# Optimization experiments

Measured on AMD Instinct MI355X. Metric: run time of the kernel, lower is better.

Reference implementation:

```python
import jax, jax.numpy as jnp
import numpy as np

B, N, C, H = 4, 1025, 768, 12
KEEP_RATIO = 0.25
BETA = 1.0


def setup_inputs() -> dict:
    key = jax.random.key(0)
    k1, k2, k3, k4, k5 = jax.random.split(key, 5)
    x = jax.random.normal(k1, (B, N, C), dtype=jnp.float32)
    ucb_count_score = jax.random.uniform(k2, (H, N), dtype=jnp.float32)
    W_qkv = jax.random.normal(k3, (C, 3 * C), dtype=jnp.float32) * 0.02
    W_proj = jax.random.normal(k4, (C, C), dtype=jnp.float32) * 0.02
    b_proj = jax.random.normal(k5, (C,), dtype=jnp.float32) * 0.02
    return {"x": x, "ucb_count_score": ucb_count_score, "W_qkv": W_qkv,
            "W_proj": W_proj, "b_proj": b_proj, "counter": 100, "ucb_enabled": 1}


def reference(x, ucb_count_score, W_qkv, W_proj, b_proj, counter, ucb_enabled):
    Bn, Nn, Cn = x.shape
    Dh = Cn // H
    scale = Dh ** -0.5
    # qkv projection (no bias, qkv_bias=False)
    qkv = (x @ W_qkv).reshape(Bn, Nn, 3, H, Dh)
    q = jnp.transpose(qkv[:, :, 0], (0, 2, 1, 3))  # [B,H,N,Dh]
    k = jnp.transpose(qkv[:, :, 1], (0, 2, 1, 3))
    v = jnp.transpose(qkv[:, :, 2], (0, 2, 1, 3))
    attn_probs = jax.nn.softmax(jnp.einsum('bhnd,bhmd->bhnm', q, k) * scale, axis=-1)

    if ucb_enabled and counter > 50:
        # UCB pruning path (exclude_cls=True, keep_ratio set)
        total_patches = Nn - 1
        k_sel = max(1, int(total_patches * KEEP_RATIO))
        patch_scores = attn_probs[:, :, :, 1:].mean(axis=2)  # [B,H,N-1]
        expl = BETA * jnp.sqrt(jnp.log(counter + 1.0) / (ucb_count_score[:, 1:] + 1e-6))  # [H,N-1]
        global_ucb = (patch_scores + expl[None]).mean(axis=1)  # [B,N-1]
        _, sel = jax.lax.top_k(global_ucb, k_sel)  # [B,k]
        tok = sel + 1  # shift for CLS
        # keep[b,j] = 1 if token j is CLS or selected in batch b
        keep = jnp.zeros((Bn, Nn), dtype=attn_probs.dtype)
        keep = keep.at[jnp.arange(Bn)[:, None], tok].set(1.0).at[:, 0].set(1.0)
        # mask[b,h,i,j] = keep[b,i] OR keep[b,j]
        mask = jnp.maximum(keep[:, None, :, None], keep[:, None, None, :])
        pruned = attn_probs * mask
        pruned = pruned / (pruned.sum(axis=-1, keepdims=True) + 1e-8)
        context = jnp.einsum('bhnm,bhmd->bhnd', pruned, v)
        cnt = jnp.zeros((Nn,), dtype=jnp.float32).at[tok.reshape(-1)].add(1.0) / Bn
        score_delta = jnp.broadcast_to(cnt[None, :], ucb_count_score.shape)
    else:
        context = jnp.einsum('bhnm,bhmd->bhnd', attn_probs, v)
        score_delta = None

    out = context.transpose(0, 2, 1, 3).reshape(Bn, Nn, Cn) @ W_proj + b_proj
    return out, score_delta
```

## Files before the change

### kernel.cpp

```cpp
#include <hip/hip_runtime.h>
#include <hip/hip_bf16.h>
#include <math.h>

#define Bb 4
#define Nn 1025
#define Cc 768
#define Hh 12
#define BH (Bb*Hh)
#define M_ROWS 4100
#define KSEL 256
#define JP 1152
#define IT_TILES 68
#define NIB 17
#define NIB32 33
#define NSW 9
#define MT16 264
#define KC24 24
#define JT16 72
#define STR4 292
#define NPART 396
#define NSCORE 1024
#define QSCALE 0.18033688011112042f

#define CAST_X_BLK 1584
#define CAST_WQKV_BLK 864
#define CAST_WPROJ_BLK 288

typedef __attribute__((ext_vector_type(8))) short short8;
typedef __attribute__((ext_vector_type(4))) short short4s;
typedef __attribute__((ext_vector_type(4))) float floatx4;

static __device__ inline unsigned short f2bf(float v) {
    __hip_bfloat16 b = __float2bfloat16(v);
    return *reinterpret_cast<unsigned short*>(&b);
}
static __device__ inline short tbfs(float f) {
    union { float f; unsigned u; } x; x.f = f;
    return (short)(x.u >> 16);
}
static __device__ inline float fexp2(float x) {
    return __builtin_amdgcn_exp2f(x);
}

static __device__ inline void async16(const unsigned short* g, unsigned short* l) {
    __builtin_amdgcn_global_load_lds(
        (const __attribute__((address_space(1))) unsigned int*)g,
        (__attribute__((address_space(3))) unsigned int*)l, 16, 0, 0);
}

__global__ __launch_bounds__(256)
void cast_all(const float* __restrict__ x, const float* __restrict__ Wqkv,
              const float* __restrict__ Wproj,
              unsigned short* __restrict__ xA, unsigned short* __restrict__ WB,
              unsigned short* __restrict__ WpB)
{
    int blk = blockIdx.x;
    int tid = threadIdx.x;
    if (blk < CAST_X_BLK) {
        int s = blk * 256 + tid;
        int ml = s & 15, q = (s >> 4) & 3;
        int t2 = s >> 6;
        int mt = t2 % MT16, kc = t2 / MT16;
        int m = mt * 16 + ml, k = kc * 32 + q * 8;
        uint4 pk = {0u, 0u, 0u, 0u};
        if (m < M_ROWS) {
            float4 a = *(const float4*)&x[(size_t)m * 768 + k];
            float4 b2 = *(const float4*)&x[(size_t)m * 768 + k + 4];
            pk.x = (unsigned)f2bf(a.x)  | ((unsigned)f2bf(a.y)  << 16);
            pk.y = (unsigned)f2bf(a.z)  | ((unsigned)f2bf(a.w)  << 16);
            pk.z = (unsigned)f2bf(b2.x) | ((unsigned)f2bf(b2.y) << 16);
            pk.w = (unsigned)f2bf(b2.z) | ((unsigned)f2bf(b2.w) << 16);
        }
        *(uint4*)&xA[(size_t)s * 8] = pk;
        return;
    }
    const float* W;
    unsigned short* WO;
    int N, NT, s;
    if (blk < CAST_X_BLK + CAST_WQKV_BLK) {
        W = Wqkv; WO = WB; N = 2304; NT = 144;
        s = (blk - CAST_X_BLK) * 256 + tid;
    } else {
        W = Wproj; WO = WpB; N = 768; NT = 48;
        s = (blk - CAST_X_BLK - CAST_WQKV_BLK) * 256 + tid;
    }
    int nl = s & 15, q = (s >> 4) & 3;
    int t2 = s >> 6;
    int nt = t2 % NT, kc = t2 / NT;
    int n = nt * 16 + nl, k = kc * 32 + q * 8;
    unsigned hv[8];
#pragma unroll
    for (int e = 0; e < 8; ++e)
        hv[e] = f2bf(W[(size_t)(k + e) * N + n]);
    uint4 pk;
    pk.x = hv[0] | (hv[1] << 16);
    pk.y = hv[2] | (hv[3] << 16);
    pk.z = hv[4] | (hv[5] << 16);
    pk.w = hv[6] | (hv[7] << 16);
    *(uint4*)&WO[(size_t)s * 8] = pk;
}

template<int NT, int MODE>
__global__ __launch_bounds__(256, 3)
void gemm_mfma(const unsigned short* __restrict__ Af,
               const unsigned short* __restrict__ Bf,
               int Nt16,
               unsigned short* __restrict__ qB, unsigned short* __restrict__ kF,
               unsigned short* __restrict__ vF,
               float* __restrict__ outp, const float* __restrict__ bias)
{
    __shared__ __align__(16) unsigned short ldsA[4096];
    __shared__ __align__(16) unsigned short ldsB[NT * 1024];
    const int tid = threadIdx.x;
    const int ln = tid & 63, w = tid >> 6;
    const int wm = w >> 1, wn = w & 1;
    const int mb = blockIdx.x, nb = blockIdx.y;

    floatx4 acc[4][NT];
#pragma unroll
    for (int mt = 0; mt < 4; ++mt)
#pragma unroll
        for (int nt = 0; nt < NT; ++nt)
            acc[mt][nt] = (floatx4){0.f, 0.f, 0.f, 0.f};

    for (int kc = 0; kc < KC24; ++kc) {
        const unsigned short* gA = Af + ((size_t)(kc * MT16 + mb * 8)) * 512;
        const unsigned short* gB = Bf + ((size_t)(kc * Nt16 + nb * (NT * 2))) * 512;
        async16(gA + (size_t)(w * 128 + ln) * 8,      &ldsA[w * 1024]);
        async16(gA + (size_t)(w * 128 + 64 + ln) * 8, &ldsA[w * 1024 + 512]);
        if (NT == 4) {
            async16(gB + (size_t)(w * 128 + ln) * 8,      &ldsB[w * 1024]);
            async16(gB + (size_t)(w * 128 + 64 + ln) * 8, &ldsB[w * 1024 + 512]);
        } else {
            async16(gB + (size_t)(w * 64 + ln) * 8, &ldsB[w * 512]);
        }
        __syncthreads();

        short8 Am[4], Bn[NT];
#pragma unroll
        for (int mt = 0; mt < 4; ++mt)
            Am[mt] = *(const short8*)&ldsA[((wm * 4 + mt) * 64 + ln) * 8];
#pragma unroll
        for (int nt = 0; nt < NT; ++nt)
            Bn[nt] = *(const short8*)&ldsB[((wn * NT + nt) * 64 + ln) * 8];
#pragma unroll
        for (int mt = 0; mt < 4; ++mt)
#pragma unroll
            for (int nt = 0; nt < NT; ++nt)
                acc[mt][nt] = __builtin_amdgcn_mfma_f32_16x16x32_bf16(
                    Am[mt], Bn[nt], acc[mt][nt], 0, 0, 0);
        __syncthreads();
    }

    const int q = ln >> 4, l15 = ln & 15;
    if (MODE == 1) {
#pragma unroll
        for (int nt = 0; nt < NT; ++nt) {
            int gn = nb * (NT * 32) + wn * (NT * 16) + nt * 16 + l15;
            float bv = bias[gn];
#pragma unroll
            for (int mt = 0; mt < 4; ++mt) {
                int gmb = mb * 128 + wm * 64 + mt * 16 + q * 4;
#pragma unroll
                for (int r = 0; r < 4; ++r) {
                    int gm = gmb + r;
                    if (gm < M_ROWS)
                        outp[(size_t)gm * 768 + gn] = acc[mt][nt][r] + bv;
                }
            }
        }
    } else {
#pragma unroll
        for (int nt = 0; nt < NT; ++nt) {
            int gn = nb * (NT * 32) + wn * (NT * 16) + nt * 16 + l15;
            int s = (gn >= 1536) ? 2 : (gn >= 768 ? 1 : 0);
            int rr = gn - s * Cc;
            int h = rr >> 6, d = rr & 63;
#pragma unroll
            for (int mt = 0; mt < 4; ++mt) {
                int gmb = mb * 128 + wm * 64 + mt * 16 + q * 4;
#pragma unroll
                for (int r = 0; r < 4; ++r) {
                    int gm = gmb + r;
                    if (gm >= M_ROWS) continue;
                    int b = gm / Nn;
                    int n = gm - b * Nn;
                    int bh = b * Hh + h;
                    float val = acc[mt][nt][r];
                    if (s == 0) {
                        int idx = (((bh * IT_TILES + (n >> 4)) * 2 + (d >> 5)) * 512)
                                  + ((((d & 31) >> 3) * 16 + (n & 15)) * 8) + (d & 7);
                        qB[idx] = f2bf(val * QSCALE);
                    } else if (s == 1) {
                        size_t idx = ((((size_t)bh * JT16 + (n >> 4)) * 2 + (d >> 5)) * 64
                                      + ((d >> 3) & 3) * 16 + (n & 15)) * 8 + (d & 7);
                        kF[idx] = f2bf(val);
                    } else {
                        size_t idx = ((((size_t)bh * JT16 + (n >> 4)) * 4 + (d >> 4)) * 64
                                      + ((n >> 2) & 3) * 16 + (d & 15)) * 4 + (n & 3);
                        vF[idx] = f2bf(val);
                    }
                }
            }
        }
    }
}

__global__ __launch_bounds__(256, 4)
void attn_colsum_mfma(const unsigned short* __restrict__ qB,
                      const unsigned short* __restrict__ kF,
                      float* __restrict__ colsum_part)
{
    __shared__ unsigned int expS8[32 * STR4];
    __shared__ float red16[16][32];
    __shared__ float linv[32];

    const int blk = blockIdx.x;
    const int x8 = blk & 7, g = blk >> 3;
    const int bh = x8 * 6 + (g % 6);
    const int ib = g / 6;
    const int tid = threadIdx.x;
    const int ws = tid >> 6;
    const int ln = tid & 63;
    const int i16 = ln & 15, q = ln >> 4;

    const unsigned short* kBase = kF + (size_t)bh * JT16 * 1024;

    short8 Qf[2][2];
#pragma unroll
    for (int it = 0; it < 2; ++it)
#pragma unroll
        for (int kc = 0; kc < 2; ++kc)
            Qf[it][kc] = *(const short8*)&qB[(((size_t)bh * IT_TILES + ib * 2 + it) * 2 + kc) * 512 + ln * 8];

    float lacc[2][2] = {{0.f, 0.f}, {0.f, 0.f}};

    short8 Kc[2][2], Kn[2][2];
#pragma unroll
    for (int jt = 0; jt < 2; ++jt)
#pragma unroll
        for (int kc = 0; kc < 2; ++kc)
            Kc[jt][kc] = *(const short8*)&kBase[(((ws * 2 + jt) * 2 + kc) * 64 + ln) * 8];

    for (int sw = 0; sw < NSW; ++sw) {
        if (sw + 1 < NSW) {
#pragma unroll
            for (int jt = 0; jt < 2; ++jt)
#pragma unroll
                for (int kc = 0; kc < 2; ++kc)
                    Kn[jt][kc] = *(const short8*)&kBase[((((sw + 1) * 8 + ws * 2 + jt) * 2 + kc) * 64 + ln) * 8];
        }

        floatx4 S[2][2];
#pragma unroll
        for (int it = 0; it < 2; ++it)
#pragma unroll
            for (int jt = 0; jt < 2; ++jt) {
                S[it][jt] = (floatx4){0.f, 0.f, 0.f, 0.f};
#pragma unroll
                for (int kc = 0; kc < 2; ++kc)
                    S[it][jt] = __builtin_amdgcn_mfma_f32_16x16x32_bf16(Kc[jt][kc], Qf[it][kc], S[it][jt], 0, 0, 0);
            }

        const int jbase0 = sw * 128 + ws * 32 + q * 4;
#pragma unroll
        for (int it = 0; it < 2; ++it) {
            const int irow = it * 16 + i16;
#pragma unroll
            for (int jt = 0; jt < 2; ++jt) {
                int jbase = jbase0 + jt * 16;
                float p[4];
#pragma unroll
                for (int r = 0; r < 4; ++r) {
                    float vld = (jbase + r < Nn) ? 1.f : 0.f;
                    p[r] = fexp2(S[it][jt][r]) * vld;
                }
                lacc[it][jt] += (p[0] + p[1]) + (p[2] + p[3]);
                unsigned u = (unsigned)__builtin_amdgcn_cvt_pk_fp8_f32(p[0], p[1], 0, false);
                u = (unsigned)__builtin_amdgcn_cvt_pk_fp8_f32(p[2], p[3], (int)u, true);
                expS8[irow * STR4 + (jbase >> 2)] = u;
            }
        }
#pragma unroll
        for (int jt = 0; jt < 2; ++jt)
#pragma unroll
            for (int kc = 0; kc < 2; ++kc)
                Kc[jt][kc] = Kn[jt][kc];
    }

    __syncthreads();
#pragma unroll
    for (int it = 0; it < 2; ++it)
        red16[ws * 4 + q][it * 16 + i16] = lacc[it][0] + lacc[it][1];
    __syncthreads();
    if (tid < 32) {
        float s = 0.f;
#pragma unroll
        for (int t = 0; t < 16; ++t) s += red16[t][tid];
        int gi = ib * 32 + tid;
        linv[tid] = (gi < Nn) ? 1.f / s : 0.f;
    }
    __syncthreads();

    float* prow = colsum_part + (size_t)(bh * NIB32 + ib) * JP;
    for (int grp = tid; grp < 288; grp += 256) {
        float a0 = 0.f, a1 = 0.f, a2 = 0.f, a3 = 0.f;
#pragma unroll 8
        for (int i = 0; i < 32; ++i) {
            unsigned v = expS8[i * STR4 + grp];
            float li = linv[i];
            a0 += __builtin_amdgcn_cvt_f32_fp8(v, 0) * li;
            a1 += __builtin_amdgcn_cvt_f32_fp8(v, 1) * li;
            a2 += __builtin_amdgcn_cvt_f32_fp8(v, 2) * li;
            a3 += __builtin_amdgcn_cvt_f32_fp8(v, 3) * li;
        }
        float4 o = {a0, a1, a2, a3};
        *(float4*)&prow[grp * 4] = o;
    }
}

__global__ __launch_bounds__(256)
void colsum_reduce(const float* __restrict__ colsum_part,
                   const float* __restrict__ ucb_score,
                   const int* __restrict__ counter_p,
                   float* __restrict__ scoreF)
{
    const int b = blockIdx.x, jc = blockIdx.y;
    const int tid = threadIdx.x;
    const int j32 = tid & 31, grp = tid >> 5;
    const int t = jc * 32 + j32 + 1;
    __shared__ float red[8][32];

    const float* pb = colsum_part + (size_t)b * NPART * JP + t;
    float a0 = 0.f, a1 = 0.f;
    int r = grp;
    for (; r + 8 < NPART; r += 16) {
        a0 += pb[(size_t)r * JP];
        a1 += pb[(size_t)(r + 8) * JP];
    }
    for (; r < NPART; r += 8) a0 += pb[(size_t)r * JP];
    red[grp][j32] = a0 + a1;
    __syncthreads();

    if (tid < 32) {
        float cs = 0.f;
#pragma unroll
        for (int g = 0; g < 8; ++g) cs += red[g][tid];
        int tt = jc * 32 + tid + 1;
        float lc = logf((float)(*counter_p) + 1.0f);
        float s = cs * (1.0f / (float)Nn);
#pragma unroll
        for (int h = 0; h < Hh; ++h)
            s += sqrtf(lc / (ucb_score[h * Nn + tt] + 1e-6f));
        s *= (1.0f / (float)Hh);
        scoreF[b * NSCORE + tt - 1] = s;
    }
}

__global__ __launch_bounds__(1024)
void ucb_topk(const float* __restrict__ scoreF,
              float* __restrict__ keepP, float* __restrict__ cnt_b)
{
    const int b = blockIdx.x;
    const int tid = threadIdx.x;
    const int w = tid >> 6, ln = tid & 63;
    __shared__ int hist[8192];
    __shared__ int wtot[16];
    __shared__ unsigned ckey[1024];
    __shared__ int cidx[1024];
    __shared__ int s_tb, s_rem, ccount;

    for (int tpos = tid; tpos < JP; tpos += 1024) {
        keepP[b * JP + tpos] = 0.f;
        cnt_b[b * JP + tpos] = 0.f;
    }

    const unsigned key = __float_as_uint(scoreF[b * NSCORE + tid]);

    for (int tpos = tid; tpos < 8192; tpos += 1024) hist[tpos] = 0;
    if (tid == 0) ccount = 0;
    __syncthreads();
    atomicAdd(&hist[key >> 18], 1);
    __syncthreads();

    int part = 0;
#pragma unroll
    for (int q2 = 0; q2 < 8; ++q2) part += hist[tid * 8 + q2];
    int v = part;
#pragma unroll
    for (int off = 1; off < 64; off <<= 1) {
        int tv = __shfl_down(v, off);
        if (ln + off < 64) v += tv;
    }
    if (ln == 0) wtot[w] = v;
    __syncthreads();
    int woff = 0;
    for (int w2 = w + 1; w2 < 16; ++w2) woff += wtot[w2];
    int cum_above = v + woff - part;
    for (int q2 = 7; q2 >= 0; --q2) {
        int c = hist[tid * 8 + q2];
        if (cum_above < KSEL && cum_above + c >= KSEL) {
            s_tb = tid * 8 + q2;
            s_rem = KSEL - cum_above;
        }
        cum_above += c;
    }
    __syncthreads();

    const int tb = s_tb, rem = s_rem;
    const int mybin = (int)(key >> 18);
    bool sel = mybin > tb;
    if (mybin == tb) {
        int p = atomicAdd(&ccount, 1);
        ckey[p] = key; cidx[p] = tid;
    }
    __syncthreads();
    if (mybin == tb) {
        int rr = 0;
        const int cc = ccount;
        for (int c = 0; c < cc; ++c) {
            unsigned kc2 = ckey[c]; int ic = cidx[c];
            if (kc2 > key || (kc2 == key && ic < tid)) ++rr;
        }
        sel = rr < rem;
    }
    if (sel) {
        int tok = tid + 1;
        keepP[b * JP + tok] = 1.f;
        cnt_b[b * JP + tok] = 1.0f / (float)Bb;
    }
    if (tid == 0) keepP[b * JP + 0] = 1.f;
}

__global__ __launch_bounds__(256, 2)
void attn_ctx_mfma(const unsigned short* __restrict__ qB,
                   const unsigned short* __restrict__ kF,
                   const unsigned short* __restrict__ vF,
                   const float* __restrict__ keepP, const float* __restrict__ cnt_b,
                   unsigned short* __restrict__ ctxA, float* __restrict__ out2)
{
    __shared__ __align__(16) char smem[25856];
    float* keeps = (float*)smem;
    float* red16 = (float*)(smem + 4608);
    float* dinv  = (float*)(smem + 8704);
    float* redC  = (float*)(smem + 8960);

    const int blk = blockIdx.x;
    const int x8 = blk & 7, g = blk >> 3;
    const int bh = x8 * 6 + (g % 6);
    const int ib = g / 6;
    const int b = bh / Hh, h = bh % Hh;
    const int tid = threadIdx.x;
    const int ws = tid >> 6;
    const int ln = tid & 63;
    const int i16 = ln & 15, q = ln >> 4;

    {
        int t = blk * 256 + tid;
        if (t < Hh * Nn) {
            int n = t % Nn;
            out2[t] = cnt_b[0 * JP + n] + cnt_b[1 * JP + n]
                    + cnt_b[2 * JP + n] + cnt_b[3 * JP + n];
        }
    }

    for (int t = tid; t < JP; t += 256) keeps[t] = keepP[b * JP + t];

    const unsigned short* kBase = kF + (size_t)bh * JT16 * 1024;
    const unsigned short* vBase = vF + (size_t)bh * JT16 * 1024;

    short8 Qf[4][2];
#pragma unroll
    for (int it = 0; it < 4; ++it)
#pragma unroll
        for (int kc = 0; kc < 2; ++kc)
            Qf[it][kc] = *(const short8*)&qB[(((size_t)bh * IT_TILES + ib * 4 + it) * 2 + kc) * 512 + ln * 8];

    __syncthreads();

    float keepi[4];
#pragma unroll
    for (int it = 0; it < 4; ++it)
        keepi[it] = keeps[(ib * 4 + it) * 16 + i16];

    floatx4 ctxacc[4][4];
#pragma unroll
    for (int it = 0; it < 4; ++it)
#pragma unroll
        for (int dt = 0; dt < 4; ++dt)
            ctxacc[it][dt] = (floatx4){0.f, 0.f, 0.f, 0.f};
    float dsacc[4] = {0.f, 0.f, 0.f, 0.f};

    short8 Kc[2][2], Kn[2][2];
    short4s Vc[2][4], Vn[2][4];
#pragma unroll
    for (int jt = 0; jt < 2; ++jt) {
#pragma unroll
        for (int kc = 0; kc < 2; ++kc)
            Kc[jt][kc] = *(const short8*)&kBase[(((ws * 2 + jt) * 2 + kc) * 64 + ln) * 8];
#pragma unroll
        for (int dt = 0; dt < 4; ++dt)
            Vc[jt][dt] = *(const short4s*)&vBase[(((ws * 2 + jt) * 4 + dt) * 64 + ln) * 4];
    }

    for (int sw = 0; sw < NSW; ++sw) {
        if (sw + 1 < NSW) {
#pragma unroll
            for (int jt = 0; jt < 2; ++jt) {
#pragma unroll
                for (int kc = 0; kc < 2; ++kc)
                    Kn[jt][kc] = *(const short8*)&kBase[((((sw + 1) * 8 + ws * 2 + jt) * 2 + kc) * 64 + ln) * 8];
#pragma unroll
                for (int dt = 0; dt < 4; ++dt)
                    Vn[jt][dt] = *(const short4s*)&vBase[((((sw + 1) * 8 + ws * 2 + jt) * 4 + dt) * 64 + ln) * 4];
            }
        }

        float kjv[2][4], vld[2][4];
#pragma unroll
        for (int jt = 0; jt < 2; ++jt)
#pragma unroll
            for (int r = 0; r < 4; ++r) {
                int jj = sw * 128 + ws * 32 + jt * 16 + q * 4 + r;
                vld[jt][r] = (jj < Nn) ? 1.f : 0.f;
                kjv[jt][r] = keeps[jj];
            }

#pragma unroll
        for (int it = 0; it < 4; ++it) {
            floatx4 S[2];
#pragma unroll
            for (int jt = 0; jt < 2; ++jt) {
                S[jt] = (floatx4){0.f, 0.f, 0.f, 0.f};
#pragma unroll
                for (int kc = 0; kc < 2; ++kc)
                    S[jt] = __builtin_amdgcn_mfma_f32_16x16x32_bf16(Kc[jt][kc], Qf[it][kc], S[jt], 0, 0, 0);
            }
            bool rk = keepi[it] > 0.5f;
#pragma unroll
            for (int jt = 0; jt < 2; ++jt) {
                float p[4];
#pragma unroll
                for (int r = 0; r < 4; ++r) {
                    float w = rk ? vld[jt][r] : kjv[jt][r];
                    p[r] = fexp2(S[jt][r]) * w;
                    dsacc[it] += p[r];
                }
                short4s Pa;
                Pa.x = tbfs(p[0]); Pa.y = tbfs(p[1]);
                Pa.z = tbfs(p[2]); Pa.w = tbfs(p[3]);
#pragma unroll
                for (int dt = 0; dt < 4; ++dt)
                    ctxacc[it][dt] = __builtin_amdgcn_mfma_f32_16x16x16bf16_1k(
                        Pa, Vc[jt][dt], ctxacc[it][dt], 0, 0, 0);
            }
        }

#pragma unroll
        for (int jt = 0; jt < 2; ++jt) {
#pragma unroll
            for (int kc = 0; kc < 2; ++kc)
                Kc[jt][kc] = Kn[jt][kc];
#pragma unroll
            for (int dt = 0; dt < 4; ++dt)
                Vc[jt][dt] = Vn[jt][dt];
        }
    }

    __syncthreads();
#pragma unroll
    for (int it = 0; it < 4; ++it) red16[(ws * 4 + q) * 64 + it * 16 + i16] = dsacc[it];
    __syncthreads();
    if (tid < 64) {
        float s = 0.f;
#pragma unroll
        for (int t = 0; t < 16; ++t) s += red16[t * 64 + tid];
        dinv[tid] = 1.f / (s + 1e-8f);
    }
    for (int w = 0; w < 4; ++w) {
        __syncthreads();
        if (ws == w) {
#pragma unroll
            for (int it = 0; it < 4; ++it)
#pragma unroll
                for (int dt = 0; dt < 4; ++dt)
#pragma unroll
                    for (int r = 0; r < 4; ++r) {
                        int i = it * 16 + q * 4 + r;
                        int d = dt * 16 + i16;
                        float v = ctxacc[it][dt][r];
                        redC[i * 66 + d] = (w == 0) ? v : (redC[i * 66 + d] + v);
                    }
        }
    }
    __syncthreads();
#pragma unroll
    for (int rep = 0; rep < 2; ++rep) {
        int s2 = tid + rep * 256;
        int i = s2 >> 3, dc = s2 & 7;
        int gi = ib * 64 + i;
        if (gi < Nn) {
            int m = b * Nn + gi;
            float dv = dinv[i];
            const float* src = &redC[i * 66 + dc * 8];
            uint4 pk;
            pk.x = (unsigned)f2bf(src[0] * dv) | ((unsigned)f2bf(src[1] * dv) << 16);
            pk.y = (unsigned)f2bf(src[2] * dv) | ((unsigned)f2bf(src[3] * dv) << 16);
            pk.z = (unsigned)f2bf(src[4] * dv) | ((unsigned)f2bf(src[5] * dv) << 16);
            pk.w = (unsigned)f2bf(src[6] * dv) | ((unsigned)f2bf(src[7] * dv) << 16);
            int kc2 = h * 2 + (dc >> 2);
            int q2 = dc & 3;
            size_t idx = (((size_t)(kc2 * MT16 + (m >> 4))) * 64 + q2 * 16 + (m & 15)) * 8;
            *(uint4*)&ctxA[idx] = pk;
        }
    }
}

extern "C" void kernel_launch(void* const* d_in, const int* in_sizes, int n_in,
                              void* d_out, int out_size, void* d_ws, size_t ws_size,
                              hipStream_t stream) {
    const float* x     = (const float*)d_in[0];
    const float* ucb   = (const float*)d_in[1];
    const float* Wqkv  = (const float*)d_in[2];
    const float* Wproj = (const float*)d_in[3];
    const float* bproj = (const float*)d_in[4];
    const int*   counter = (const int*)d_in[5];

    unsigned short* qB = (unsigned short*)d_ws;
    unsigned short* kF = qB + 3342336;
    unsigned short* vF = kF + 3538944;
    float* keepP    = (float*)(vF + 3538944);
    float* cnt_b    = keepP + 4608;
    unsigned short* ctxA = (unsigned short*)(cnt_b + 4608);
    unsigned short* xA   = ctxA + 3244032;
    unsigned short* WB   = xA + 3244032;
    unsigned short* WpB  = WB + 1769472;
    float* colsum_part = (float*)(WpB + 589824);
    float* scoreF = colsum_part + 1824768;

    float* out  = (float*)d_out;
    float* out2 = out + 3148800;

    cast_all<<<dim3(CAST_X_BLK + CAST_WQKV_BLK + CAST_WPROJ_BLK), dim3(256), 0, stream>>>(
        x, Wqkv, Wproj, xA, WB, WpB);
    gemm_mfma<4, 0><<<dim3(33, 18), dim3(256), 0, stream>>>(
        xA, WB, 144, qB, kF, vF, nullptr, nullptr);
    attn_colsum_mfma<<<dim3(8 * 198), dim3(256), 0, stream>>>(qB, kF, colsum_part);
    colsum_reduce<<<dim3(Bb, 32), dim3(256), 0, stream>>>(colsum_part, ucb, counter, scoreF);
    ucb_topk<<<dim3(Bb), dim3(1024), 0, stream>>>(scoreF, keepP, cnt_b);
    attn_ctx_mfma<<<dim3(8 * 102), dim3(256), 0, stream>>>(qB, kF, vF, keepP, cnt_b, ctxA, out2);
    gemm_mfma<2, 1><<<dim3(33, 12), dim3(256), 0, stream>>>(
        ctxA, WpB, 48, nullptr, nullptr, nullptr, out, bproj);
}
```

Before: 200.5 us.

## Use 16x16x32 MFMA for P·V with permlane-swapped P fragments

The P·V product moves from two 16x16x16 bf16 MFMAs per d-tile to a single 16x16x32 MFMA. To do this, V is stored in a new 32-row tiled layout, and the probability fragments are repacked across lanes with v_permlane32/16_swap instructions. This halves the number of MFMA issues and widens the V loads to 16 bytes. In exchange it depends on the permlane swap producing exactly the operand layout the MFMA expects, and adds a few cross-lane instructions per tile.

```diff
diff --git a/kernel.cpp b/kernel.cpp
--- a/kernel.cpp
+++ b/kernel.cpp
@@ -17,6 +17,7 @@
 #define MT16 264
 #define KC24 24
 #define JT16 72
+#define JT32 36
 #define STR4 292
 #define NPART 396
 #define NSCORE 1024
@@ -29,17 +30,19 @@
 typedef __attribute__((ext_vector_type(8))) short short8;
 typedef __attribute__((ext_vector_type(4))) short short4s;
 typedef __attribute__((ext_vector_type(4))) float floatx4;
+typedef __attribute__((ext_vector_type(4))) unsigned uintx4;
 
 static __device__ inline unsigned short f2bf(float v) {
     __hip_bfloat16 b = __float2bfloat16(v);
     return *reinterpret_cast<unsigned short*>(&b);
 }
-static __device__ inline short tbfs(float f) {
-    union { float f; unsigned u; } x; x.f = f;
-    return (short)(x.u >> 16);
-}
 static __device__ inline float fexp2(float x) {
     return __builtin_amdgcn_exp2f(x);
+}
+static __device__ inline unsigned pkbf(float lo, float hi) {
+    union { float f; unsigned u; } a, b;
+    a.f = lo; b.f = hi;
+    return (a.u >> 16) | (b.u & 0xffff0000u);
 }
 
 static __device__ inline void async16(const unsigned short* g, unsigned short* l) {
@@ -196,8 +199,8 @@
                                       + ((d >> 3) & 3) * 16 + (n & 15)) * 8 + (d & 7);
                         kF[idx] = f2bf(val);
                     } else {
-                        size_t idx = ((((size_t)bh * JT16 + (n >> 4)) * 4 + (d >> 4)) * 64
-                                      + ((n >> 2) & 3) * 16 + (d & 15)) * 4 + (n & 3);
+                        size_t idx = ((((size_t)bh * JT32 + (n >> 5)) * 4 + (d >> 4)) * 64
+                                      + ((n >> 3) & 3) * 16 + (d & 15)) * 8 + (n & 7);
                         vF[idx] = f2bf(val);
                     }
                 }
@@ -467,7 +470,7 @@
     for (int t = tid; t < JP; t += 256) keeps[t] = keepP[b * JP + t];
 
     const unsigned short* kBase = kF + (size_t)bh * JT16 * 1024;
-    const unsigned short* vBase = vF + (size_t)bh * JT16 * 1024;
+    const unsigned short* vBase = vF + (size_t)bh * JT32 * 2048;
 
     short8 Qf[4][2];
 #pragma unroll
@@ -492,28 +495,26 @@
     float dsacc[4] = {0.f, 0.f, 0.f, 0.f};
 
     short8 Kc[2][2], Kn[2][2];
-    short4s Vc[2][4], Vn[2][4];
-#pragma unroll
-    for (int jt = 0; jt < 2; ++jt) {
+    short8 Vc8[4], Vn8[4];
+#pragma unroll
+    for (int jt = 0; jt < 2; ++jt)
 #pragma unroll
         for (int kc = 0; kc < 2; ++kc)
             Kc[jt][kc] = *(const short8*)&kBase[(((ws * 2 + jt) * 2 + kc) * 64 + ln) * 8];
 #pragma unroll
-        for (int dt = 0; dt < 4; ++dt)
-            Vc[jt][dt] = *(const short4s*)&vBase[(((ws * 2 + jt) * 4 + dt) * 64 + ln) * 4];
-    }
+    for (int dt = 0; dt < 4; ++dt)
+        Vc8[dt] = *(const short8*)&vBase[(((size_t)ws * 4 + dt) * 64 + ln) * 8];
 
     for (int sw = 0; sw < NSW; ++sw) {
         if (sw + 1 < NSW) {
 #pragma unroll
-            for (int jt = 0; jt < 2; ++jt) {
+            for (int jt = 0; jt < 2; ++jt)
 #pragma unroll
                 for (int kc = 0; kc < 2; ++kc)
                     Kn[jt][kc] = *(const short8*)&kBase[((((sw + 1) * 8 + ws * 2 + jt) * 2 + kc) * 64 + ln) * 8];
 #pragma unroll
-                for (int dt = 0; dt < 4; ++dt)
-                    Vn[jt][dt] = *(const short4s*)&vBase[((((sw + 1) * 8 + ws * 2 + jt) * 4 + dt) * 64 + ln) * 4];
-            }
+            for (int dt = 0; dt < 4; ++dt)
+                Vn8[dt] = *(const short8*)&vBase[((((size_t)(sw + 1) * 4 + ws) * 4 + dt) * 64 + ln) * 8];
         }
 
         float kjv[2][4], vld[2][4];
@@ -537,34 +538,38 @@
                     S[jt] = __builtin_amdgcn_mfma_f32_16x16x32_bf16(Kc[jt][kc], Qf[it][kc], S[jt], 0, 0, 0);
             }
             bool rk = keepi[it] > 0.5f;
-#pragma unroll
-            for (int jt = 0; jt < 2; ++jt) {
-                float p[4];
+            float p[2][4];
+#pragma unroll
+            for (int jt = 0; jt < 2; ++jt)
 #pragma unroll
                 for (int r = 0; r < 4; ++r) {
                     float w = rk ? vld[jt][r] : kjv[jt][r];
-                    p[r] = fexp2(S[jt][r]) * w;
-                    dsacc[it] += p[r];
+                    p[jt][r] = fexp2(S[jt][r]) * w;
+                    dsacc[it] += p[jt][r];
                 }
-                short4s Pa;
-                Pa.x = tbfs(p[0]); Pa.y = tbfs(p[1]);
-                Pa.z = tbfs(p[2]); Pa.w = tbfs(p[3]);
-#pragma unroll
-                for (int dt = 0; dt < 4; ++dt)
-                    ctxacc[it][dt] = __builtin_amdgcn_mfma_f32_16x16x16bf16_1k(
-                        Pa, Vc[jt][dt], ctxacc[it][dt], 0, 0, 0);
-            }
-        }
-
-#pragma unroll
-        for (int jt = 0; jt < 2; ++jt) {
+            unsigned Au = pkbf(p[0][0], p[0][1]);
+            unsigned Bu = pkbf(p[0][2], p[0][3]);
+            unsigned Cu = pkbf(p[1][0], p[1][1]);
+            unsigned Du = pkbf(p[1][2], p[1][3]);
+            asm("v_permlane32_swap_b32 %0, %1" : "+v"(Au), "+v"(Cu));
+            asm("v_permlane32_swap_b32 %0, %1" : "+v"(Bu), "+v"(Du));
+            asm("v_permlane16_swap_b32 %0, %1" : "+v"(Au), "+v"(Cu));
+            asm("v_permlane16_swap_b32 %0, %1" : "+v"(Bu), "+v"(Du));
+            short8 Wf = __builtin_bit_cast(short8, (uintx4){Au, Bu, Cu, Du});
+#pragma unroll
+            for (int dt = 0; dt < 4; ++dt)
+                ctxacc[it][dt] = __builtin_amdgcn_mfma_f32_16x16x32_bf16(
+                    Wf, Vc8[dt], ctxacc[it][dt], 0, 0, 0);
+        }
+
+#pragma unroll
+        for (int jt = 0; jt < 2; ++jt)
 #pragma unroll
             for (int kc = 0; kc < 2; ++kc)
                 Kc[jt][kc] = Kn[jt][kc];
 #pragma unroll
-            for (int dt = 0; dt < 4; ++dt)
-                Vc[jt][dt] = Vn[jt][dt];
-        }
+        for (int dt = 0; dt < 4; ++dt)
+            Vc8[dt] = Vn8[dt];
     }
 
     __syncthreads();
```

After: 201.1 us. Within noise of the previous version (+0.3%).
